# Kernel tuning notes

Hardware: AMD Instinct MI355X
Metric: run time of the kernel (lower is better)

## Reference

```python
import jax, jax.numpy as jnp
import numpy as np

B, S, N_WIRES, EMBED_DIM, NUM_HEADS = 4, 2048, 8, 512, 8
D_K = EMBED_DIM // NUM_HEADS


def setup_inputs() -> dict:
    key = jax.random.key(0)
    k_x, k_th, k_q, k_k, k_v, k_c = jax.random.split(key, 6)
    x = jax.random.normal(k_x, (B, S, N_WIRES), dtype=jnp.float32)
    # trainable RX rotation angles, one per wire
    theta = jax.random.normal(k_th, (N_WIRES,), dtype=jnp.float32) * 0.1
    # nn.Linear(n_wires, embed_dim, bias=False) weights have shape (embed_dim, n_wires)
    sc_in = 1.0 / np.sqrt(N_WIRES)
    Wq = jax.random.normal(k_q, (EMBED_DIM, N_WIRES), dtype=jnp.float32) * sc_in
    Wk = jax.random.normal(k_k, (EMBED_DIM, N_WIRES), dtype=jnp.float32) * sc_in
    Wv = jax.random.normal(k_v, (EMBED_DIM, N_WIRES), dtype=jnp.float32) * sc_in
    Wc = jax.random.normal(k_c, (EMBED_DIM, EMBED_DIM), dtype=jnp.float32) * (1.0 / np.sqrt(EMBED_DIM))
    return {"x": x, "theta": theta, "Wq": Wq, "Wk": Wk, "Wv": Wv, "Wc": Wc}


def reference(x, theta, Wq, Wk, Wv, Wc):
    # Quantum encoding closed form: RX(x_i) then RX(theta_i) on |0> per wire gives <Z> = cos(x_i + theta_i).
    proj = jnp.cos(x + theta)  # (B, S, n_wires)
    b, s, _ = proj.shape
    q = jnp.einsum('bsn,en->bse', proj, Wq)
    k = jnp.einsum('bsn,en->bse', proj, Wk)
    v = jnp.einsum('bsn,en->bse', proj, Wv)
    # split heads: (B, H, S, d_k)
    q = q.reshape(b, s, NUM_HEADS, D_K).transpose(0, 2, 1, 3)
    k = k.reshape(b, s, NUM_HEADS, D_K).transpose(0, 2, 1, 3)
    v = v.reshape(b, s, NUM_HEADS, D_K).transpose(0, 2, 1, 3)
    scores = jnp.einsum('bhqd,bhkd->bhqk', q, k) / np.sqrt(D_K).astype(np.float32)
    attn = jax.nn.softmax(scores, axis=-1)  # dropout is identity at inference
    out = jnp.einsum('bhqk,bhkd->bhqd', attn, v)
    out = out.transpose(0, 2, 1, 3).reshape(b, s, EMBED_DIM)
    return jnp.einsum('bse,fe->bsf', out, Wc)
```

## Files before the change

### kernel.cpp

```cpp
#include <hip/hip_runtime.h>
#include <stdint.h>

#define N_B 4
#define S_LEN 2048
#define N_H 8
#define E_DIM 512

typedef __attribute__((ext_vector_type(8))) short bf16x8;
typedef __attribute__((ext_vector_type(4))) float f32x4;
typedef __attribute__((ext_vector_type(4))) unsigned int u32x4;
typedef __attribute__((ext_vector_type(2))) unsigned int u32x2;
typedef __attribute__((ext_vector_type(4))) unsigned short u16x4;
typedef __attribute__((ext_vector_type(8))) unsigned short u16x8;

#define MFMA16(a, b, c) __builtin_amdgcn_mfma_f32_16x16x32_bf16((a), (b), (c), 0, 0, 0)

__device__ __forceinline__ unsigned short f2bf(float f) {
    union { float f; unsigned int u; } v; v.f = f;
    unsigned int r = v.u + 0x7fffu + ((v.u >> 16) & 1u);
    return (unsigned short)(r >> 16);
}

__device__ __forceinline__ unsigned int pack2bf(float lo, float hi) {
    union { float f; unsigned int u; } a, b; a.f = lo; b.f = hi;
    return __builtin_amdgcn_perm(b.u + 0x8000u, a.u + 0x8000u, 0x07060302u);
}

__device__ __forceinline__ float fexp2(float x) {
#if __has_builtin(__builtin_amdgcn_exp2f)
    return __builtin_amdgcn_exp2f(x);
#else
    return exp2f(x);
#endif
}

#define Q_SCALE 0.18033688f

__global__ __launch_bounds__(256) void qkv_kernel(
    const float* __restrict__ x, const float* __restrict__ theta,
    const float* __restrict__ Wq, const float* __restrict__ Wk,
    const float* __restrict__ Wv,
    unsigned short* __restrict__ Q, unsigned short* __restrict__ K,
    unsigned short* __restrict__ Vt)
{
    __shared__ float proj[32][8];
    const int tid = threadIdx.x;
    const int mat = blockIdx.x % 3;
    const int chunk = blockIdx.x / 3;
    const int row0 = chunk * 32;
    const int b = row0 >> 11;
    const int s_in_b = row0 & (S_LEN - 1);

    proj[tid >> 3][tid & 7] = cosf(x[row0 * 8 + tid] + theta[tid & 7]);
    __syncthreads();

    if (mat < 2) {
        const float* W = (mat == 0) ? Wq : Wk;
        const float scale = (mat == 0) ? Q_SCALE : 1.0f;
        unsigned short* outp = (mat == 0) ? Q : K;
        const int eg = (tid & 127) * 4;
        const int sg = (tid >> 7) * 16;
        float w[4][8];
        #pragma unroll
        for (int e = 0; e < 4; ++e)
            #pragma unroll
            for (int n = 0; n < 8; ++n)
                w[e][n] = W[(eg + e) * 8 + n] * scale;
        const int h = eg >> 6, d0 = eg & 63;
        unsigned short* p0 = outp + ((size_t)(b * N_H + h) * S_LEN + s_in_b + sg) * 64 + d0;
        #pragma unroll 4
        for (int s = 0; s < 16; ++s) {
            f32x4 pa = *(const f32x4*)&proj[sg + s][0];
            f32x4 pc = *(const f32x4*)&proj[sg + s][4];
            u16x4 o;
            #pragma unroll
            for (int e = 0; e < 4; ++e) {
                float a = 0.f;
                #pragma unroll
                for (int n = 0; n < 4; ++n)
                    a += pa[n] * w[e][n] + pc[n] * w[e][n + 4];
                o[e] = f2bf(a);
            }
            *(u16x4*)&p0[s * 64] = o;
        }
    } else {
        f32x4 ps[8][2];
        const int sl0 = (tid & 3) * 8;
        #pragma unroll
        for (int k2 = 0; k2 < 8; ++k2) {
            ps[k2][0] = *(const f32x4*)&proj[sl0 + k2][0];
            ps[k2][1] = *(const f32x4*)&proj[sl0 + k2][4];
        }
        const int ecol = tid >> 2;
        for (int pass = 0; pass < 8; ++pass) {
            const int e = pass * 64 + ecol;
            const int h = e >> 6, dd = e & 63;
            float wr[8];
            #pragma unroll
            for (int n = 0; n < 8; ++n) wr[n] = Wv[e * 8 + n];
            u16x8 pk;
            #pragma unroll
            for (int k2 = 0; k2 < 8; ++k2) {
                float acc = 0.f;
                #pragma unroll
                for (int n = 0; n < 4; ++n)
                    acc += ps[k2][0][n] * wr[n] + ps[k2][1][n] * wr[n + 4];
                pk[k2] = f2bf(acc);
            }
            *(u16x8*)&Vt[((size_t)(b * N_H + h) * 64 + dd) * S_LEN + s_in_b + sl0] = pk;
        }
    }
}

__global__ __launch_bounds__(256, 4) void flash_kernel(
    const unsigned short* __restrict__ Q, const unsigned short* __restrict__ K,
    const unsigned short* __restrict__ Vt,
    float* __restrict__ OP, float* __restrict__ LS)
{
    __shared__ short kt[64 * 72];
    __shared__ short pb[128 * 72];

    const int tid = threadIdx.x;
    const int lane = tid & 63, w = tid >> 6;
    const int quad = lane >> 4, lq = lane & 15;
    const int kh = blockIdx.x & 1;
    const int qt = (blockIdx.x >> 1) & 15;
    const int bh = blockIdx.x >> 5;

    const unsigned short* Qb = Q + (size_t)bh * S_LEN * 64;
    const unsigned short* Kb = K + ((size_t)bh * S_LEN + kh * 1024) * 64;
    const unsigned short* Vb = Vt + (size_t)bh * 64 * S_LEN + kh * 1024;

    bf16x8 qf[2][2];
    #pragma unroll
    for (int mt = 0; mt < 2; ++mt)
        #pragma unroll
        for (int ks = 0; ks < 2; ++ks)
            qf[mt][ks] = *(const bf16x8*)&Qb[(size_t)(qt * 128 + w * 32 + mt * 16 + lq) * 64 + ks * 32 + quad * 8];

    f32x4 oacc[2][4];
    #pragma unroll
    for (int mt = 0; mt < 2; ++mt)
        #pragma unroll
        for (int dt = 0; dt < 4; ++dt) oacc[mt][dt] = 0.f;
    float lsum[2] = {0.f, 0.f};

    u32x4 pkr[2];
    #pragma unroll
    for (int i = 0; i < 2; ++i) {
        const int u = tid + (i << 8);
        pkr[i] = *(const u32x4*)&Kb[(size_t)(u >> 3) * 64 + (u & 7) * 8];
    }

    for (int kti = 0; kti < 16; ++kti) {
        __syncthreads();
        #pragma unroll
        for (int i = 0; i < 2; ++i) {
            const int u = tid + (i << 8);
            *(u32x4*)&kt[(u >> 3) * 72 + (u & 7) * 8] = pkr[i];
        }
        __syncthreads();

        const int kb = kti * 64;
        const int kb2 = (kti < 15) ? kb + 64 : 0;
        #pragma unroll
        for (int i = 0; i < 2; ++i) {
            const int u = tid + (i << 8);
            pkr[i] = *(const u32x4*)&Kb[(size_t)(kb2 + (u >> 3)) * 64 + (u & 7) * 8];
        }

        f32x4 sacc[2][4];
        #pragma unroll
        for (int mt = 0; mt < 2; ++mt)
            #pragma unroll
            for (int mts = 0; mts < 4; ++mts) sacc[mt][mts] = 0.f;
        #pragma unroll
        for (int mts = 0; mts < 4; ++mts) {
            #pragma unroll
            for (int ks = 0; ks < 2; ++ks) {
                bf16x8 af = *(const bf16x8*)&kt[(mts * 16 + lq) * 72 + ks * 32 + quad * 8];
                sacc[0][mts] = MFMA16(af, qf[0][ks], sacc[0][mts]);
                sacc[1][mts] = MFMA16(af, qf[1][ks], sacc[1][mts]);
            }
        }

        #pragma unroll
        for (int mt = 0; mt < 2; ++mt) {
            #pragma unroll
            for (int mts = 0; mts < 4; ++mts) {
                f32x4 p;
                #pragma unroll
                for (int e = 0; e < 4; ++e) p[e] = fexp2(sacc[mt][mts][e]);
                lsum[mt] += (p[0] + p[1]) + (p[2] + p[3]);
                u32x2 pw = { pack2bf(p[0], p[1]), pack2bf(p[2], p[3]) };
                *(u32x2*)&pb[(w * 32 + mt * 16 + lq) * 72 + mts * 16 + quad * 4] = pw;
            }
        }

        #pragma unroll
        for (int ks = 0; ks < 2; ++ks) {
            bf16x8 af0 = *(const bf16x8*)&pb[(w * 32 + lq) * 72 + ks * 32 + quad * 8];
            bf16x8 af1 = *(const bf16x8*)&pb[(w * 32 + 16 + lq) * 72 + ks * 32 + quad * 8];
            #pragma unroll
            for (int dt = 0; dt < 4; ++dt) {
                bf16x8 bf = *(const bf16x8*)&Vb[(size_t)(dt * 16 + lq) * S_LEN + kb + ks * 32 + quad * 8];
                oacc[0][dt] = MFMA16(af0, bf, oacc[0][dt]);
                oacc[1][dt] = MFMA16(af1, bf, oacc[1][dt]);
            }
        }
    }

    float* OPb = OP + ((size_t)(kh * 32 + bh) * S_LEN + qt * 128) * 64;
    float* LSb = LS + ((size_t)(kh * 32 + bh) * S_LEN + qt * 128);
    #pragma unroll
    for (int mt = 0; mt < 2; ++mt) {
        float rs = lsum[mt];
        rs += __shfl_xor(rs, 16);
        rs += __shfl_xor(rs, 32);
        if (quad == 0) LSb[w * 32 + mt * 16 + lq] = rs;
        #pragma unroll
        for (int dt = 0; dt < 4; ++dt)
            #pragma unroll
            for (int r = 0; r < 4; ++r)
                OPb[(size_t)(w * 32 + mt * 16 + quad * 4 + r) * 64 + dt * 16 + lq] = oacc[mt][dt][r];
    }
}

__global__ __launch_bounds__(256) void combine_kernel(
    const float* __restrict__ OP, const float* __restrict__ LS,
    unsigned short* __restrict__ O)
{
    const int t = blockIdx.x * 256 + threadIdx.x;
    const int bhq = t >> 2;
    const int dg = (t & 3) << 4;
    const int bh = bhq >> 11, q = bhq & 2047;
    const int b = bh >> 3, h = bh & 7;
    const float ls = LS[(size_t)bh * S_LEN + q] + LS[(size_t)(32 + bh) * S_LEN + q];
    const float inv = 1.0f / ls;
    const float* p0 = OP + ((size_t)bh * S_LEN + q) * 64 + dg;
    const float* p1 = OP + ((size_t)(32 + bh) * S_LEN + q) * 64 + dg;
    unsigned short* dst = O + ((size_t)b * S_LEN + q) * E_DIM + h * 64 + dg;
    #pragma unroll
    for (int c = 0; c < 4; ++c) {
        f32x4 a = *(const f32x4*)&p0[c * 4];
        f32x4 bb = *(const f32x4*)&p1[c * 4];
        u16x4 o = { f2bf((a[0] + bb[0]) * inv), f2bf((a[1] + bb[1]) * inv),
                    f2bf((a[2] + bb[2]) * inv), f2bf((a[3] + bb[3]) * inv) };
        *(u16x4*)&dst[c * 4] = o;
    }
}

__global__ __launch_bounds__(256, 4) void outproj_kernel(
    const unsigned short* __restrict__ O, const float* __restrict__ Wc,
    float* __restrict__ Y)
{
    __shared__ short at[64 * 72];
    __shared__ short bt[64 * 72];
    const int tid = threadIdx.x;
    const int lane = tid & 63, w = tid >> 6;
    const int quad = lane >> 4, lq = lane & 15;
    const int m0 = (blockIdx.x >> 3) * 64;
    const int f0 = (blockIdx.x & 7) * 64;

    f32x4 acc[4];
    #pragma unroll
    for (int nt = 0; nt < 4; ++nt) acc[nt] = 0.f;

    u32x4 pa[2];
    f32x4 pw[4];
    #pragma unroll
    for (int i = 0; i < 2; ++i) {
        const int u = tid + (i << 8);
        pa[i] = *(const u32x4*)&O[(size_t)(m0 + (u >> 3)) * E_DIM + (u & 7) * 8];
    }
    #pragma unroll
    for (int i = 0; i < 4; ++i) {
        const int u = tid + (i << 8);
        pw[i] = *(const f32x4*)&Wc[(size_t)(f0 + (u >> 4)) * E_DIM + (u & 15) * 4];
    }

    for (int e0 = 0; e0 < E_DIM; e0 += 64) {
        __syncthreads();
        #pragma unroll
        for (int i = 0; i < 2; ++i) {
            const int u = tid + (i << 8);
            *(u32x4*)&at[(u >> 3) * 72 + (u & 7) * 8] = pa[i];
        }
        #pragma unroll
        for (int i = 0; i < 4; ++i) {
            const int u = tid + (i << 8);
            u16x4 pk = { f2bf(pw[i][0]), f2bf(pw[i][1]), f2bf(pw[i][2]), f2bf(pw[i][3]) };
            *(u16x4*)&bt[(u >> 4) * 72 + (u & 15) * 4] = pk;
        }
        __syncthreads();

        const int e1 = (e0 + 64 < E_DIM) ? e0 + 64 : 0;
        #pragma unroll
        for (int i = 0; i < 2; ++i) {
            const int u = tid + (i << 8);
            pa[i] = *(const u32x4*)&O[(size_t)(m0 + (u >> 3)) * E_DIM + e1 + (u & 7) * 8];
        }
        #pragma unroll
        for (int i = 0; i < 4; ++i) {
            const int u = tid + (i << 8);
            pw[i] = *(const f32x4*)&Wc[(size_t)(f0 + (u >> 4)) * E_DIM + e1 + (u & 15) * 4];
        }

        bf16x8 afk[2];
        #pragma unroll
        for (int ks = 0; ks < 2; ++ks)
            afk[ks] = *(const bf16x8*)&at[(w * 16 + lq) * 72 + ks * 32 + quad * 8];
        #pragma unroll
        for (int nt = 0; nt < 4; ++nt) {
            #pragma unroll
            for (int ks = 0; ks < 2; ++ks) {
                bf16x8 bf = *(const bf16x8*)&bt[(nt * 16 + lq) * 72 + ks * 32 + quad * 8];
                acc[nt] = MFMA16(afk[ks], bf, acc[nt]);
            }
        }
    }

    #pragma unroll
    for (int nt = 0; nt < 4; ++nt)
        #pragma unroll
        for (int r = 0; r < 4; ++r)
            Y[(size_t)(m0 + w * 16 + quad * 4 + r) * E_DIM + f0 + nt * 16 + lq] = acc[nt][r];
}

extern "C" void kernel_launch(void* const* d_in, const int* in_sizes, int n_in,
                              void* d_out, int out_size, void* d_ws, size_t ws_size,
                              hipStream_t stream) {
    const float* x     = (const float*)d_in[0];
    const float* theta = (const float*)d_in[1];
    const float* Wq    = (const float*)d_in[2];
    const float* Wk    = (const float*)d_in[3];
    const float* Wv    = (const float*)d_in[4];
    const float* Wc    = (const float*)d_in[5];
    float* Y = (float*)d_out;

    char* ws = (char*)d_ws;
    unsigned short* Q  = (unsigned short*)(ws);
    unsigned short* K  = (unsigned short*)(ws + ((size_t)8 << 20));
    unsigned short* Vt = (unsigned short*)(ws + ((size_t)16 << 20));
    float*          OP = (float*)(ws + ((size_t)24 << 20));
    float*          LS = (float*)(ws + ((size_t)56 << 20));
    unsigned short* O  = Q;

    qkv_kernel<<<(N_B * S_LEN / 32) * 3, 256, 0, stream>>>(x, theta, Wq, Wk, Wv, Q, K, Vt);
    flash_kernel<<<N_B * N_H * (S_LEN / 128) * 2, 256, 0, stream>>>(Q, K, Vt, OP, LS);
    combine_kernel<<<(N_B * N_H * S_LEN * 4) / 256, 256, 0, stream>>>(OP, LS, O);
    outproj_kernel<<<(N_B * S_LEN / 64) * (E_DIM / 64), 256, 0, stream>>>(O, Wc, Y);
}
```

Measured before the change: 169.0 us.

## Stage V tiles in LDS and use 2 waves with 64 query rows each

The flash kernel now runs 128-thread blocks where each wave handles 64 query rows instead of 32. V tiles are prefetched into registers and staged in shared memory alongside K, replacing the direct global reads of V inside the PV loop. The LDS row stride changes from 72 to 68 shorts in both kernels, which changes the bank-conflict pattern. Each LDS-loaded K/V fragment is reused across more MFMAs, at the cost of more accumulator registers and half as many waves per block, which may lower occupancy.

```diff
diff --git a/kernel.cpp b/kernel.cpp
--- a/kernel.cpp
+++ b/kernel.cpp
@@ -14,6 +14,8 @@
 typedef __attribute__((ext_vector_type(8))) unsigned short u16x8;
 
 #define MFMA16(a, b, c) __builtin_amdgcn_mfma_f32_16x16x32_bf16((a), (b), (c), 0, 0, 0)
+
+#define LSTR 68
 
 __device__ __forceinline__ unsigned short f2bf(float f) {
     union { float f; unsigned int u; } v; v.f = f;
@@ -112,13 +114,14 @@
     }
 }
 
-__global__ __launch_bounds__(256, 4) void flash_kernel(
+__global__ __launch_bounds__(128, 2) void flash_kernel(
     const unsigned short* __restrict__ Q, const unsigned short* __restrict__ K,
     const unsigned short* __restrict__ Vt,
     float* __restrict__ OP, float* __restrict__ LS)
 {
-    __shared__ short kt[64 * 72];
-    __shared__ short pb[128 * 72];
+    __shared__ short kt[64 * LSTR];
+    __shared__ short vt[64 * LSTR];
+    __shared__ short pb[128 * LSTR];
 
     const int tid = threadIdx.x;
     const int lane = tid & 63, w = tid >> 6;
@@ -131,61 +134,64 @@
     const unsigned short* Kb = K + ((size_t)bh * S_LEN + kh * 1024) * 64;
     const unsigned short* Vb = Vt + (size_t)bh * 64 * S_LEN + kh * 1024;
 
-    bf16x8 qf[2][2];
-    #pragma unroll
-    for (int mt = 0; mt < 2; ++mt)
+    bf16x8 qf[4][2];
+    #pragma unroll
+    for (int mt = 0; mt < 4; ++mt)
         #pragma unroll
         for (int ks = 0; ks < 2; ++ks)
-            qf[mt][ks] = *(const bf16x8*)&Qb[(size_t)(qt * 128 + w * 32 + mt * 16 + lq) * 64 + ks * 32 + quad * 8];
-
-    f32x4 oacc[2][4];
-    #pragma unroll
-    for (int mt = 0; mt < 2; ++mt)
+            qf[mt][ks] = *(const bf16x8*)&Qb[(size_t)(qt * 128 + w * 64 + mt * 16 + lq) * 64 + ks * 32 + quad * 8];
+
+    f32x4 oacc[4][4];
+    #pragma unroll
+    for (int mt = 0; mt < 4; ++mt)
         #pragma unroll
         for (int dt = 0; dt < 4; ++dt) oacc[mt][dt] = 0.f;
-    float lsum[2] = {0.f, 0.f};
-
-    u32x4 pkr[2];
-    #pragma unroll
-    for (int i = 0; i < 2; ++i) {
-        const int u = tid + (i << 8);
+    float lsum[4] = {0.f, 0.f, 0.f, 0.f};
+
+    u32x4 pkr[4], pvr[4];
+    #pragma unroll
+    for (int i = 0; i < 4; ++i) {
+        const int u = tid + (i << 7);
         pkr[i] = *(const u32x4*)&Kb[(size_t)(u >> 3) * 64 + (u & 7) * 8];
+        pvr[i] = *(const u32x4*)&Vb[(size_t)(u >> 3) * S_LEN + (u & 7) * 8];
     }
 
     for (int kti = 0; kti < 16; ++kti) {
         __syncthreads();
         #pragma unroll
-        for (int i = 0; i < 2; ++i) {
-            const int u = tid + (i << 8);
-            *(u32x4*)&kt[(u >> 3) * 72 + (u & 7) * 8] = pkr[i];
+        for (int i = 0; i < 4; ++i) {
+            const int u = tid + (i << 7);
+            *(u32x4*)&kt[(u >> 3) * LSTR + (u & 7) * 8] = pkr[i];
+            *(u32x4*)&vt[(u >> 3) * LSTR + (u & 7) * 8] = pvr[i];
         }
         __syncthreads();
 
-        const int kb = kti * 64;
-        const int kb2 = (kti < 15) ? kb + 64 : 0;
-        #pragma unroll
-        for (int i = 0; i < 2; ++i) {
-            const int u = tid + (i << 8);
+        const int kb2 = (kti < 15) ? (kti + 1) * 64 : 0;
+        #pragma unroll
+        for (int i = 0; i < 4; ++i) {
+            const int u = tid + (i << 7);
             pkr[i] = *(const u32x4*)&Kb[(size_t)(kb2 + (u >> 3)) * 64 + (u & 7) * 8];
-        }
-
-        f32x4 sacc[2][4];
-        #pragma unroll
-        for (int mt = 0; mt < 2; ++mt)
+            pvr[i] = *(const u32x4*)&Vb[(size_t)(u >> 3) * S_LEN + kb2 + (u & 7) * 8];
+        }
+
+        f32x4 sacc[4][4];
+        #pragma unroll
+        for (int mt = 0; mt < 4; ++mt)
             #pragma unroll
             for (int mts = 0; mts < 4; ++mts) sacc[mt][mts] = 0.f;
         #pragma unroll
         for (int mts = 0; mts < 4; ++mts) {
             #pragma unroll
             for (int ks = 0; ks < 2; ++ks) {
-                bf16x8 af = *(const bf16x8*)&kt[(mts * 16 + lq) * 72 + ks * 32 + quad * 8];
-                sacc[0][mts] = MFMA16(af, qf[0][ks], sacc[0][mts]);
-                sacc[1][mts] = MFMA16(af, qf[1][ks], sacc[1][mts]);
-            }
-        }
-
-        #pragma unroll
-        for (int mt = 0; mt < 2; ++mt) {
+                bf16x8 af = *(const bf16x8*)&kt[(mts * 16 + lq) * LSTR + ks * 32 + quad * 8];
+                #pragma unroll
+                for (int mt = 0; mt < 4; ++mt)
+                    sacc[mt][mts] = MFMA16(af, qf[mt][ks], sacc[mt][mts]);
+            }
+        }
+
+        #pragma unroll
+        for (int mt = 0; mt < 4; ++mt) {
             #pragma unroll
             for (int mts = 0; mts < 4; ++mts) {
                 f32x4 p;
@@ -193,19 +199,22 @@
                 for (int e = 0; e < 4; ++e) p[e] = fexp2(sacc[mt][mts][e]);
                 lsum[mt] += (p[0] + p[1]) + (p[2] + p[3]);
                 u32x2 pw = { pack2bf(p[0], p[1]), pack2bf(p[2], p[3]) };
-                *(u32x2*)&pb[(w * 32 + mt * 16 + lq) * 72 + mts * 16 + quad * 4] = pw;
+                *(u32x2*)&pb[(w * 64 + mt * 16 + lq) * LSTR + mts * 16 + quad * 4] = pw;
             }
         }
 
         #pragma unroll
         for (int ks = 0; ks < 2; ++ks) {
-            bf16x8 af0 = *(const bf16x8*)&pb[(w * 32 + lq) * 72 + ks * 32 + quad * 8];
-            bf16x8 af1 = *(const bf16x8*)&pb[(w * 32 + 16 + lq) * 72 + ks * 32 + quad * 8];
+            bf16x8 af[4];
+            #pragma unroll
+            for (int mt = 0; mt < 4; ++mt)
+                af[mt] = *(const bf16x8*)&pb[(w * 64 + mt * 16 + lq) * LSTR + ks * 32 + quad * 8];
             #pragma unroll
             for (int dt = 0; dt < 4; ++dt) {
-                bf16x8 bf = *(const bf16x8*)&Vb[(size_t)(dt * 16 + lq) * S_LEN + kb + ks * 32 + quad * 8];
-                oacc[0][dt] = MFMA16(af0, bf, oacc[0][dt]);
-                oacc[1][dt] = MFMA16(af1, bf, oacc[1][dt]);
+                bf16x8 bf = *(const bf16x8*)&vt[(dt * 16 + lq) * LSTR + ks * 32 + quad * 8];
+                #pragma unroll
+                for (int mt = 0; mt < 4; ++mt)
+                    oacc[mt][dt] = MFMA16(af[mt], bf, oacc[mt][dt]);
             }
         }
     }
@@ -213,16 +222,16 @@
     float* OPb = OP + ((size_t)(kh * 32 + bh) * S_LEN + qt * 128) * 64;
     float* LSb = LS + ((size_t)(kh * 32 + bh) * S_LEN + qt * 128);
     #pragma unroll
-    for (int mt = 0; mt < 2; ++mt) {
+    for (int mt = 0; mt < 4; ++mt) {
         float rs = lsum[mt];
         rs += __shfl_xor(rs, 16);
         rs += __shfl_xor(rs, 32);
-        if (quad == 0) LSb[w * 32 + mt * 16 + lq] = rs;
+        if (quad == 0) LSb[w * 64 + mt * 16 + lq] = rs;
         #pragma unroll
         for (int dt = 0; dt < 4; ++dt)
             #pragma unroll
             for (int r = 0; r < 4; ++r)
-                OPb[(size_t)(w * 32 + mt * 16 + quad * 4 + r) * 64 + dt * 16 + lq] = oacc[mt][dt][r];
+                OPb[(size_t)(w * 64 + mt * 16 + quad * 4 + r) * 64 + dt * 16 + lq] = oacc[mt][dt][r];
     }
 }
 
@@ -254,8 +263,8 @@
     const unsigned short* __restrict__ O, const float* __restrict__ Wc,
     float* __restrict__ Y)
 {
-    __shared__ short at[64 * 72];
-    __shared__ short bt[64 * 72];
+    __shared__ short at[64 * LSTR];
+    __shared__ short bt[64 * LSTR];
     const int tid = threadIdx.x;
     const int lane = tid & 63, w = tid >> 6;
     const int quad = lane >> 4, lq = lane & 15;
@@ -284,13 +293,13 @@
         #pragma unroll
         for (int i = 0; i < 2; ++i) {
             const int u = tid + (i << 8);
-            *(u32x4*)&at[(u >> 3) * 72 + (u & 7) * 8] = pa[i];
+            *(u32x4*)&at[(u >> 3) * LSTR + (u & 7) * 8] = pa[i];
         }
         #pragma unroll
         for (int i = 0; i < 4; ++i) {
             const int u = tid + (i << 8);
             u16x4 pk = { f2bf(pw[i][0]), f2bf(pw[i][1]), f2bf(pw[i][2]), f2bf(pw[i][3]) };
-            *(u16x4*)&bt[(u >> 4) * 72 + (u & 15) * 4] = pk;
+            *(u16x4*)&bt[(u >> 4) * LSTR + (u & 15) * 4] = pk;
         }
         __syncthreads();
 
@@ -309,12 +318,12 @@
         bf16x8 afk[2];
         #pragma unroll
         for (int ks = 0; ks < 2; ++ks)
-            afk[ks] = *(const bf16x8*)&at[(w * 16 + lq) * 72 + ks * 32 + quad * 8];
+            afk[ks] = *(const bf16x8*)&at[(w * 16 + lq) * LSTR + ks * 32 + quad * 8];
         #pragma unroll
         for (int nt = 0; nt < 4; ++nt) {
             #pragma unroll
             for (int ks = 0; ks < 2; ++ks) {
-                bf16x8 bf = *(const bf16x8*)&bt[(nt * 16 + lq) * 72 + ks * 32 + quad * 8];
+                bf16x8 bf = *(const bf16x8*)&bt[(nt * 16 + lq) * LSTR + ks * 32 + quad * 8];
                 acc[nt] = MFMA16(afk[ks], bf, acc[nt]);
             }
         }
@@ -347,7 +356,7 @@
     unsigned short* O  = Q;
 
     qkv_kernel<<<(N_B * S_LEN / 32) * 3, 256, 0, stream>>>(x, theta, Wq, Wk, Wv, Q, K, Vt);
-    flash_kernel<<<N_B * N_H * (S_LEN / 128) * 2, 256, 0, stream>>>(Q, K, Vt, OP, LS);
+    flash_kernel<<<N_B * N_H * (S_LEN / 128) * 2, 128, 0, stream>>>(Q, K, Vt, OP, LS);
     combine_kernel<<<(N_B * N_H * S_LEN * 4) / 256, 256, 0, stream>>>(OP, LS, O);
     outproj_kernel<<<(N_B * S_LEN / 64) * (E_DIM / 64), 256, 0, stream>>>(O, Wc, Y);
 }
```

Measured after the change: 144.3 us. 14.6% less time.
